# Kernel tuning notes

Hardware: AMD Instinct MI355X
Metric: run time of the kernel (lower is better)

## Reference

```python
import jax, jax.numpy as jnp
import numpy as np

N_NODES = 100000


def gcn_conv(x, edge_index, W, b):
    """PyG-style GCNConv: h = D^-1/2 (A+I) D^-1/2 (x W) + b."""
    n = x.shape[0]
    loop = jnp.arange(n)
    src = jnp.concatenate([edge_index[0], loop])  # [E+N]
    dst = jnp.concatenate([edge_index[1], loop])  # [E+N]
    # degree computed on destination nodes (PyG gcn_norm with self-loops)
    deg = jnp.zeros((n,), x.dtype).at[dst].add(1.0)
    dinv = jnp.where(deg > 0, jax.lax.rsqrt(deg), 0.0)
    norm = dinv[src] * dinv[dst]  # [E+N]
    h = x @ W  # [n, out]
    msg = h[src] * norm[:, None]  # gather + scale
    out = jax.ops.segment_sum(msg, dst, num_segments=n)  # scatter-add
    return out + b


def setup_inputs() -> dict:
    key = jax.random.key(0)
    ks = jax.random.split(key, 8)
    F_in, H, C = 64, 64, 32
    x = jax.random.normal(ks[0], (N_NODES, F_in), dtype=jnp.float32)
    edge_index = jax.random.randint(ks[1], (2, 1200000), 0, N_NODES, dtype=jnp.int64)
    W1 = jax.random.normal(ks[2], (F_in, H), dtype=jnp.float32) / np.sqrt(F_in)
    b1 = jnp.zeros((H,), jnp.float32)
    W2 = jax.random.normal(ks[3], (H, H), dtype=jnp.float32) / np.sqrt(H)
    b2 = jnp.zeros((H,), jnp.float32)
    Wc = jax.random.normal(ks[4], (H, C), dtype=jnp.float32) / np.sqrt(H)
    bc = jnp.zeros((C,), jnp.float32)
    return {"x": x, "edge_index": edge_index, "W1": W1, "b1": b1,
            "W2": W2, "b2": b2, "Wc": Wc, "bc": bc}


def reference(x, edge_index, W1, b1, W2, b2, Wc, bc):
    h = jnp.tanh(gcn_conv(x, edge_index, W1, b1))
    h = jnp.tanh(gcn_conv(h, edge_index, W2, b2))
    out = h @ Wc + bc
    return (out, h)
```

## Files before the change

### kernel.cpp

```cpp
#include <hip/hip_runtime.h>
#include <hip/hip_bf16.h>
#include <stdint.h>

#define CB_SHIFT 8
#define CB_NODES 256
#define CAP 3584
#define NBINS 512
#define PT 4096

static __device__ inline uint16_t f2bf(float f) {
    union { float f; uint32_t u; } v; v.f = f;
    uint32_t r = v.u + 0x7FFFu + ((v.u >> 16) & 1u);
    return (uint16_t)(r >> 16);
}
static __device__ inline float bflo(uint32_t u) {
    union { uint32_t u; float f; } v; v.u = u << 16; return v.f;
}
static __device__ inline float bfhi(uint32_t u) {
    union { uint32_t u; float f; } v; v.u = u & 0xFFFF0000u; return v.f;
}
static __device__ inline float bfu(uint16_t u) {
    union { uint32_t u; float f; } v; v.u = ((uint32_t)u) << 16; return v.f;
}
static __device__ inline float tanh_fast(float x) {
    x = fminf(fmaxf(x, -20.f), 20.f);
    float e = __expf(2.f * x);
    return fmaf(-2.f, __builtin_amdgcn_rcpf(e + 1.f), 1.f);
}

__global__ __launch_bounds__(256) void k_init(const uint32_t* __restrict__ e, int E,
                                              int* __restrict__ flag, int* __restrict__ gcur,
                                              int* __restrict__ dhist) {
    int t = threadIdx.x;
    dhist[t] = 0;
    gcur[t] = 0;
    gcur[256 + t] = 0;
    if (t < 64) {
        int cnt = E < 1024 ? E : 1024;
        int nz = 0;
        for (int i = t; i < cnt; i += 64) nz |= (e[2 * i + 1] != 0u);
        int any = __any(nz);
        if (t == 0) *flag = any ? 0 : 1;
    }
}

__global__ __launch_bounds__(256) void k_part(const uint32_t* __restrict__ e, int E,
                                              const int* __restrict__ flag,
                                              int* __restrict__ gcur,
                                              uint32_t* __restrict__ parts) {
    __shared__ int sh_hist[NBINS], sh_off[NBINS], sh_base[NBINS], pw[4];
    __shared__ uint32_t sh_buf[PT];
    __shared__ uint16_t sh_bkt[PT];
    int t = threadIdx.x;
    int tile0 = blockIdx.x * PT;
    int is64 = *flag;
    sh_hist[t] = 0;
    sh_hist[256 + t] = 0;
    __syncthreads();

    uint32_t rec[16]; int cb[16], rank[16];
    const uint2* e2p = (const uint2*)e;
    for (int j = 0; j < 16; ++j) {
        int idx = tile0 + j * 256 + t;
        cb[j] = -1;
        if (idx < E) {
            uint32_t s, d;
            if (is64) { s = e2p[idx].x; d = e2p[E + idx].x; }
            else      { s = e[idx];     d = e[E + idx]; }
            rec[j] = (s << CB_SHIFT) | (d & (CB_NODES - 1));
            cb[j] = (int)(d >> CB_SHIFT);
            rank[j] = atomicAdd(&sh_hist[cb[j]], 1);
        }
    }
    __syncthreads();
    int c0 = sh_hist[2 * t], c1 = sh_hist[2 * t + 1];
    int s2 = c0 + c1;
    int incl = s2;
    {
        int lane = t & 63;
        for (int o = 1; o < 64; o <<= 1) {
            int v = __shfl_up(incl, o);
            if (lane >= o) incl += v;
        }
        if (lane == 63) pw[t >> 6] = incl;
    }
    __syncthreads();
    if (t == 0) {
        int r = 0;
        for (int k = 0; k < 4; ++k) { int v = pw[k]; pw[k] = r; r += v; }
    }
    __syncthreads();
    {
        int ex = pw[t >> 6] + incl - s2;
        sh_off[2 * t] = ex;
        sh_off[2 * t + 1] = ex + c0;
        sh_base[2 * t]     = c0 ? atomicAdd(&gcur[2 * t], c0) : 0;
        sh_base[2 * t + 1] = c1 ? atomicAdd(&gcur[2 * t + 1], c1) : 0;
    }
    __syncthreads();
    for (int j = 0; j < 16; ++j) {
        if (cb[j] >= 0) {
            int slot = sh_off[cb[j]] + rank[j];
            sh_buf[slot] = rec[j];
            sh_bkt[slot] = (uint16_t)cb[j];
        }
    }
    __syncthreads();
    int total = min(PT, E - tile0);
    for (int i = t; i < total; i += 256) {
        int b = sh_bkt[i];
        int dest = sh_base[b] + (i - sh_off[b]);
        parts[(size_t)b * CAP + dest] = sh_buf[i];
    }
}

__global__ __launch_bounds__(512) void k_build(const uint32_t* __restrict__ parts,
                                               const int* __restrict__ gcur,
                                               float* __restrict__ dinv,
                                               int* __restrict__ rowbeg,
                                               int* __restrict__ rowend,
                                               uint32_t* __restrict__ col,
                                               int* __restrict__ dhist, int N) {
    __shared__ int hist[CB_NODES], cur[CB_NODES], dh[256], wsum4[4];
    __shared__ uint32_t sbuf[CAP];
    int t = threadIdx.x, cb = blockIdx.x;
    if (t < 256) { hist[t] = 0; dh[t] = 0; }
    __syncthreads();
    int cnt = gcur[cb];
    const uint32_t* rp = parts + (size_t)cb * CAP;
    for (int i = t; i < cnt; i += 512) atomicAdd(&hist[rp[i] & (CB_NODES - 1)], 1);
    __syncthreads();
    int h = 0, incl = 0;
    if (t < 256) {
        h = hist[t];
        int lane = t & 63;
        incl = h;
        for (int o = 1; o < 64; o <<= 1) {
            int v = __shfl_up(incl, o);
            if (lane >= o) incl += v;
        }
        if (lane == 63) wsum4[t >> 6] = incl;
    }
    __syncthreads();
    if (t == 0) {
        int r = 0;
        for (int k = 0; k < 4; ++k) { int v = wsum4[k]; wsum4[k] = r; r += v; }
    }
    __syncthreads();
    if (t < 256) {
        int ex = wsum4[t >> 6] + incl - h;
        cur[t] = ex;
        int n = cb * CB_NODES + t;
        int base = cb * CAP;
        if (n < N) {
            rowbeg[n] = base + ex;
            rowend[n] = base + ex + h;
            dinv[n] = rsqrtf((float)(h + 1));
            atomicAdd(&dh[min(h, 255)], 1);
        }
    }
    __syncthreads();
    if (t < 256 && dh[t]) atomicAdd(&dhist[t], dh[t]);
    for (int i = t; i < cnt; i += 512) {
        uint32_t rec = rp[i];
        int pos = atomicAdd(&cur[rec & (CB_NODES - 1)], 1);
        sbuf[pos] = rec >> CB_SHIFT;
    }
    __syncthreads();
    int base = cb * CAP;
    for (int i = t; i < cnt; i += 512) col[base + i] = sbuf[i];
}

__global__ __launch_bounds__(256) void k_dscan(const int* __restrict__ dhist,
                                               int* __restrict__ dcur) {
    __shared__ int sd[256];
    int t = threadIdx.x;
    int v = dhist[t];
    sd[t] = v; __syncthreads();
    for (int o = 1; o < 256; o <<= 1) {
        int x = (t >= o) ? sd[t - o] : 0;
        __syncthreads();
        sd[t] += x;
        __syncthreads();
    }
    dcur[t] = sd[t] - v;
}

__global__ __launch_bounds__(1024) void k_dperm(const int* __restrict__ rowbeg,
                                                const int* __restrict__ rowend,
                                                const float* __restrict__ dinv,
                                                int* __restrict__ dcur,
                                                int4* __restrict__ perm4, int N) {
    __shared__ int lh[256], lbase[256];
    int t = threadIdx.x;
    if (t < 256) lh[t] = 0;
    __syncthreads();
    int n = blockIdx.x * 1024 + t;
    int c = 0, rank = 0, beg = 0, deg = 0;
    if (n < N) {
        beg = rowbeg[n];
        deg = rowend[n] - beg;
        c = min(deg, 255);
        rank = atomicAdd(&lh[c], 1);
    }
    __syncthreads();
    if (t < 256 && lh[t]) lbase[t] = atomicAdd(&dcur[t], lh[t]);
    __syncthreads();
    if (n < N) {
        int pos = lbase[c] + rank;
        perm4[(N - 1) - pos] = make_int4(beg, deg, n, __float_as_int(dinv[n]));
    }
}

template<int ABF16>
__global__ __launch_bounds__(256) void k_gemm(const void* __restrict__ Ap,
                                              const float* __restrict__ W,
                                              const float* __restrict__ dinv,
                                              uint16_t* __restrict__ out, int N) {
    __shared__ __align__(16) float xT[64 * 68];
    __shared__ __align__(16) float Wl[64 * 64];
    int t = threadIdx.x;
#pragma unroll
    for (int j = 0; j < 16; ++j) Wl[j * 256 + t] = W[j * 256 + t];
    int n0 = blockIdx.x * 64;
    int nvalid = min(64, N - n0);
#pragma unroll
    for (int j = 0; j < 4; ++j) {
        int flat = j * 256 + t;
        int node = flat >> 4;
        int k4 = (flat & 15) * 4;
        float4 v = make_float4(0.f, 0.f, 0.f, 0.f);
        if (node < nvalid) {
            if (ABF16) {
                ushort4 u = *((const ushort4*)Ap + ((size_t)(n0 + node) * 16 + (k4 >> 2)));
                v = make_float4(bfu(u.x), bfu(u.y), bfu(u.z), bfu(u.w));
            } else {
                v = *(const float4*)((const float*)Ap + (size_t)(n0 + node) * 64 + k4);
            }
        }
        xT[(k4 + 0) * 68 + node] = v.x;
        xT[(k4 + 1) * 68 + node] = v.y;
        xT[(k4 + 2) * 68 + node] = v.z;
        xT[(k4 + 3) * 68 + node] = v.w;
    }
    __syncthreads();
    int ng = t >> 4, cg = t & 15;
    float acc[4][4] = {};
#pragma unroll 8
    for (int k = 0; k < 64; ++k) {
        float4 a = *(const float4*)&xT[k * 68 + 4 * ng];
        float4 b = *(const float4*)&Wl[k * 64 + 4 * cg];
        float av[4] = {a.x, a.y, a.z, a.w};
        float bv[4] = {b.x, b.y, b.z, b.w};
#pragma unroll
        for (int i = 0; i < 4; ++i)
#pragma unroll
            for (int j = 0; j < 4; ++j) acc[i][j] = fmaf(av[i], bv[j], acc[i][j]);
    }
#pragma unroll
    for (int i = 0; i < 4; ++i) {
        int ln = 4 * ng + i;
        if (ln < nvalid) {
            int n = n0 + ln;
            float dv = dinv[n];
            ushort4 o;
            o.x = f2bf(acc[i][0] * dv);
            o.y = f2bf(acc[i][1] * dv);
            o.z = f2bf(acc[i][2] * dv);
            o.w = f2bf(acc[i][3] * dv);
            *(ushort4*)&out[(size_t)n * 64 + 4 * cg] = o;
        }
    }
}

template<int OBF16>
__global__ __launch_bounds__(512) void k_agg(const uint16_t* __restrict__ h,
                                             const int4* __restrict__ perm4,
                                             const uint32_t* __restrict__ col,
                                             const float* __restrict__ bias,
                                             void* __restrict__ out, int N) {
    int t = threadIdx.x;
    int lane = t & 63, wid = t >> 6;
    int sub  = (lane >> 3) & 1;
    int g = lane & 7;
    const uint4* hp = (const uint4*)h;
    float bv[4];
#pragma unroll
    for (int j = 0; j < 4; ++j) bv[j] = bias[g * 8 + sub * 4 + j];
    int slot = lane >> 4;
    int idx = (blockIdx.x * 8 + wid) * 4 + slot;
    bool valid = idx < N;
    int4 pi = make_int4(0, 0, 0, 0);
    if (valid) pi = perm4[idx];
    int rs = pi.x, deg = valid ? pi.y : 0, n = pi.z;
    float di = __int_as_float(pi.w);
    int m = deg;
#pragma unroll
    for (int o = 1; o < 64; o <<= 1) m = max(m, __shfl_xor(m, o));
    int trips = (m + 1) >> 1;
    float acc[8] = {};
#pragma unroll 8
    for (int it = 0; it < trips; ++it) {
        int e = 2 * it + sub;
        if (e < deg) {
            int src = (int)col[rs + e];
            uint4 v = hp[(size_t)src * 8 + g];
            acc[0] += bflo(v.x); acc[1] += bfhi(v.x);
            acc[2] += bflo(v.y); acc[3] += bfhi(v.y);
            acc[4] += bflo(v.z); acc[5] += bfhi(v.z);
            acc[6] += bflo(v.w); acc[7] += bfhi(v.w);
        }
    }
#pragma unroll
    for (int j = 0; j < 8; ++j) acc[j] += __shfl_xor(acc[j], 8);
    if (valid) {
        float s0 = sub ? acc[4] : acc[0];
        float s1 = sub ? acc[5] : acc[1];
        float s2 = sub ? acc[6] : acc[2];
        float s3 = sub ? acc[7] : acc[3];
        uint2 v = *(const uint2*)&h[(size_t)n * 64 + g * 8 + sub * 4];
        float hn0 = bflo(v.x), hn1 = bfhi(v.x), hn2 = bflo(v.y), hn3 = bfhi(v.y);
        float r0 = tanh_fast(di * (s0 + hn0) + bv[0]);
        float r1 = tanh_fast(di * (s1 + hn1) + bv[1]);
        float r2 = tanh_fast(di * (s2 + hn2) + bv[2]);
        float r3 = tanh_fast(di * (s3 + hn3) + bv[3]);
        if (OBF16) {
            ushort4 ob;
            ob.x = f2bf(r0); ob.y = f2bf(r1); ob.z = f2bf(r2); ob.w = f2bf(r3);
            *(ushort4*)&((uint16_t*)out)[(size_t)n * 64 + g * 8 + sub * 4] = ob;
        } else {
            __align__(16) float o[4] = {r0, r1, r2, r3};
            *(float4*)&((float*)out)[(size_t)n * 64 + g * 8 + sub * 4] = *(float4*)&o[0];
        }
    }
}

__global__ __launch_bounds__(256) void k_cls(const float* __restrict__ A,
                                             const float* __restrict__ W,
                                             const float* __restrict__ bc,
                                             float* __restrict__ out, int N) {
    __shared__ __align__(16) float xT[64 * 68];
    __shared__ __align__(16) float Wl[64 * 32];
    int t = threadIdx.x;
#pragma unroll
    for (int j = 0; j < 8; ++j) Wl[j * 256 + t] = W[j * 256 + t];
    int n0 = blockIdx.x * 64;
    int nvalid = min(64, N - n0);
#pragma unroll
    for (int j = 0; j < 4; ++j) {
        int flat = j * 256 + t;
        int node = flat >> 4;
        int k4 = (flat & 15) * 4;
        float4 v = make_float4(0.f, 0.f, 0.f, 0.f);
        if (node < nvalid) v = *(const float4*)&A[(size_t)(n0 + node) * 64 + k4];
        xT[(k4 + 0) * 68 + node] = v.x;
        xT[(k4 + 1) * 68 + node] = v.y;
        xT[(k4 + 2) * 68 + node] = v.z;
        xT[(k4 + 3) * 68 + node] = v.w;
    }
    __syncthreads();
    int ng = t >> 4, cg = t & 15;
    float acc[4][2] = {};
#pragma unroll 8
    for (int k = 0; k < 64; ++k) {
        float4 a = *(const float4*)&xT[k * 68 + 4 * ng];
        float2 b = *(const float2*)&Wl[k * 32 + 2 * cg];
        float av[4] = {a.x, a.y, a.z, a.w};
#pragma unroll
        for (int i = 0; i < 4; ++i) {
            acc[i][0] = fmaf(av[i], b.x, acc[i][0]);
            acc[i][1] = fmaf(av[i], b.y, acc[i][1]);
        }
    }
    float2 bcv = *(const float2*)&bc[2 * cg];
#pragma unroll
    for (int i = 0; i < 4; ++i) {
        int ln = 4 * ng + i;
        if (ln < nvalid) {
            int n = n0 + ln;
            float2 o = make_float2(acc[i][0] + bcv.x, acc[i][1] + bcv.y);
            *(float2*)&out[(size_t)n * 32 + 2 * cg] = o;
        }
    }
}

extern "C" void kernel_launch(void* const* d_in, const int* in_sizes, int n_in,
                              void* d_out, int out_size, void* d_ws, size_t ws_size,
                              hipStream_t stream) {
    const float*    x     = (const float*)d_in[0];
    const uint32_t* edges = (const uint32_t*)d_in[1];
    const float*    W1    = (const float*)d_in[2];
    const float*    b1    = (const float*)d_in[3];
    const float*    W2    = (const float*)d_in[4];
    const float*    b2    = (const float*)d_in[5];
    const float*    Wc    = (const float*)d_in[6];
    const float*    bc    = (const float*)d_in[7];

    const int N   = in_sizes[0] / 64;
    const int E   = in_sizes[1] / 2;
    const int NBC = (N + CB_NODES - 1) >> CB_SHIFT;
    const int NTG = (N + 63) / 64;
    const int NTP = (E + PT - 1) / PT;
    const int NAG = (N + 31) / 32;
    const int NDP = (N + 1023) / 1024;

    char* w = (char*)d_ws;
    size_t off = 0;
    auto alloc = [&](size_t bytes) {
        void* p = w + off;
        off = (off + bytes + 255) & ~(size_t)255;
        return p;
    };
    int*      flag   = (int*)alloc(4);
    int*      gcur   = (int*)alloc(NBINS * 4);
    int*      dhist  = (int*)alloc(256 * 4);
    int*      dcur   = (int*)alloc(256 * 4);
    float*    dinv   = (float*)alloc((size_t)N * 4);
    uint32_t* parts  = (uint32_t*)alloc((size_t)NBC * CAP * 4);
    uint32_t* col    = (uint32_t*)alloc((size_t)NBC * CAP * 4);
    int*      rowbeg = (int*)alloc((size_t)N * 4);
    int*      rowend = (int*)alloc((size_t)N * 4);
    uint16_t* bufA   = (uint16_t*)alloc((size_t)N * 64 * 2);
    uint16_t* bufB   = (uint16_t*)alloc((size_t)N * 64 * 2);
    int4*     perm4  = (int4*)parts;

    float* outc = (float*)d_out;
    float* hfin = outc + (size_t)N * 32;

    hipLaunchKernelGGL(k_init, dim3(1), dim3(256), 0, stream, edges, E, flag, gcur, dhist);
    hipLaunchKernelGGL(k_part, dim3(NTP), dim3(256), 0, stream, edges, E, flag, gcur, parts);
    hipLaunchKernelGGL(k_build, dim3(NBC), dim3(512), 0, stream, parts, gcur, dinv, rowbeg, rowend, col, dhist, N);
    hipLaunchKernelGGL(k_dscan, dim3(1), dim3(256), 0, stream, dhist, dcur);
    hipLaunchKernelGGL(k_dperm, dim3(NDP), dim3(1024), 0, stream, rowbeg, rowend, dinv, dcur, perm4, N);

    hipLaunchKernelGGL(HIP_KERNEL_NAME(k_gemm<0>), dim3(NTG), dim3(256), 0, stream,
                       (const void*)x, W1, dinv, bufA, N);
    hipLaunchKernelGGL(HIP_KERNEL_NAME(k_agg<1>), dim3(NAG), dim3(512), 0, stream,
                       bufA, perm4, col, b1, (void*)bufB, N);
    hipLaunchKernelGGL(HIP_KERNEL_NAME(k_gemm<1>), dim3(NTG), dim3(256), 0, stream,
                       (const void*)bufB, W2, dinv, bufA, N);
    hipLaunchKernelGGL(HIP_KERNEL_NAME(k_agg<0>), dim3(NAG), dim3(512), 0, stream,
                       bufA, perm4, col, b2, (void*)hfin, N);
    hipLaunchKernelGGL(k_cls, dim3(NTG), dim3(256), 0, stream, hfin, Wc, bc, outc, N);
}
```

Baseline: 243.7 us.

## Fuse classifier matmul into second aggregation kernel and widen partition blocks

The separate classifier kernel is removed. The second aggregation kernel now stages each node's final tanh output in shared memory and computes the 64x32 classifier product with bias directly, using Wc loaded into LDS. This avoids re-reading the N x 64 fp32 hidden output from global memory and saves one launch, at the cost of extra LDS use and per-block Wc loads. Separately, the edge partition kernel moves to 512 threads with one histogram bin per thread and a two-level shuffle scan.

Result: faster. 236.2 us (-3.1%).

```diff
diff --git a/kernel.cpp b/kernel.cpp
--- a/kernel.cpp
+++ b/kernel.cpp
@@ -44,24 +44,24 @@
     }
 }
 
-__global__ __launch_bounds__(256) void k_part(const uint32_t* __restrict__ e, int E,
+__global__ __launch_bounds__(512) void k_part(const uint32_t* __restrict__ e, int E,
                                               const int* __restrict__ flag,
                                               int* __restrict__ gcur,
                                               uint32_t* __restrict__ parts) {
-    __shared__ int sh_hist[NBINS], sh_off[NBINS], sh_base[NBINS], pw[4];
+    __shared__ int sh_hist[NBINS], sh_off[NBINS], sh_base[NBINS], pw[8];
     __shared__ uint32_t sh_buf[PT];
     __shared__ uint16_t sh_bkt[PT];
     int t = threadIdx.x;
     int tile0 = blockIdx.x * PT;
     int is64 = *flag;
     sh_hist[t] = 0;
-    sh_hist[256 + t] = 0;
-    __syncthreads();
-
-    uint32_t rec[16]; int cb[16], rank[16];
+    __syncthreads();
+
+    uint32_t rec[8]; int cb[8], rank[8];
     const uint2* e2p = (const uint2*)e;
-    for (int j = 0; j < 16; ++j) {
-        int idx = tile0 + j * 256 + t;
+#pragma unroll
+    for (int j = 0; j < 8; ++j) {
+        int idx = tile0 + j * 512 + t;
         cb[j] = -1;
         if (idx < E) {
             uint32_t s, d;
@@ -73,32 +73,34 @@
         }
     }
     __syncthreads();
-    int c0 = sh_hist[2 * t], c1 = sh_hist[2 * t + 1];
-    int s2 = c0 + c1;
-    int incl = s2;
+    int c = sh_hist[t];
+    int lane = t & 63, w = t >> 6;
+    int incl = c;
+    for (int o = 1; o < 64; o <<= 1) {
+        int v = __shfl_up(incl, o);
+        if (lane >= o) incl += v;
+    }
+    if (lane == 63) pw[w] = incl;
+    __syncthreads();
+    if (t < 8) {
+        int v = pw[t];
+        int inc2 = v;
+#pragma unroll
+        for (int o = 1; o < 8; o <<= 1) {
+            int u = __shfl_up(inc2, o);
+            if (t >= o) inc2 += u;
+        }
+        pw[t] = inc2 - v;
+    }
+    __syncthreads();
     {
-        int lane = t & 63;
-        for (int o = 1; o < 64; o <<= 1) {
-            int v = __shfl_up(incl, o);
-            if (lane >= o) incl += v;
-        }
-        if (lane == 63) pw[t >> 6] = incl;
-    }
-    __syncthreads();
-    if (t == 0) {
-        int r = 0;
-        for (int k = 0; k < 4; ++k) { int v = pw[k]; pw[k] = r; r += v; }
-    }
-    __syncthreads();
-    {
-        int ex = pw[t >> 6] + incl - s2;
-        sh_off[2 * t] = ex;
-        sh_off[2 * t + 1] = ex + c0;
-        sh_base[2 * t]     = c0 ? atomicAdd(&gcur[2 * t], c0) : 0;
-        sh_base[2 * t + 1] = c1 ? atomicAdd(&gcur[2 * t + 1], c1) : 0;
-    }
-    __syncthreads();
-    for (int j = 0; j < 16; ++j) {
+        int ex = pw[w] + incl - c;
+        sh_off[t] = ex;
+        sh_base[t] = c ? atomicAdd(&gcur[t], c) : 0;
+    }
+    __syncthreads();
+#pragma unroll
+    for (int j = 0; j < 8; ++j) {
         if (cb[j] >= 0) {
             int slot = sh_off[cb[j]] + rank[j];
             sh_buf[slot] = rec[j];
@@ -107,7 +109,7 @@
     }
     __syncthreads();
     int total = min(PT, E - tile0);
-    for (int i = t; i < total; i += 256) {
+    for (int i = t; i < total; i += 512) {
         int b = sh_bkt[i];
         int dest = sh_base[b] + (i - sh_off[b]);
         parts[(size_t)b * CAP + dest] = sh_buf[i];
@@ -273,13 +275,23 @@
     }
 }
 
-template<int OBF16>
+template<int OBF16, int CLS>
 __global__ __launch_bounds__(512) void k_agg(const uint16_t* __restrict__ h,
                                              const int4* __restrict__ perm4,
                                              const uint32_t* __restrict__ col,
                                              const float* __restrict__ bias,
-                                             void* __restrict__ out, int N) {
-    int t = threadIdx.x;
+                                             void* __restrict__ out,
+                                             const float* __restrict__ Wc,
+                                             const float* __restrict__ bc,
+                                             float* __restrict__ outc, int N) {
+    __shared__ __align__(16) float WcL[CLS ? 64 * 32 : 1];
+    __shared__ __align__(16) float hstage[CLS ? 8 : 1][4][64];
+    int t = threadIdx.x;
+    if (CLS) {
+#pragma unroll
+        for (int j = 0; j < 4; ++j) WcL[j * 512 + t] = Wc[j * 512 + t];
+        __syncthreads();
+    }
     int lane = t & 63, wid = t >> 6;
     int sub  = (lane >> 3) & 1;
     int g = lane & 7;
@@ -332,54 +344,28 @@
             __align__(16) float o[4] = {r0, r1, r2, r3};
             *(float4*)&((float*)out)[(size_t)n * 64 + g * 8 + sub * 4] = *(float4*)&o[0];
         }
-    }
-}
-
-__global__ __launch_bounds__(256) void k_cls(const float* __restrict__ A,
-                                             const float* __restrict__ W,
-                                             const float* __restrict__ bc,
-                                             float* __restrict__ out, int N) {
-    __shared__ __align__(16) float xT[64 * 68];
-    __shared__ __align__(16) float Wl[64 * 32];
-    int t = threadIdx.x;
-#pragma unroll
-    for (int j = 0; j < 8; ++j) Wl[j * 256 + t] = W[j * 256 + t];
-    int n0 = blockIdx.x * 64;
-    int nvalid = min(64, N - n0);
-#pragma unroll
-    for (int j = 0; j < 4; ++j) {
-        int flat = j * 256 + t;
-        int node = flat >> 4;
-        int k4 = (flat & 15) * 4;
-        float4 v = make_float4(0.f, 0.f, 0.f, 0.f);
-        if (node < nvalid) v = *(const float4*)&A[(size_t)(n0 + node) * 64 + k4];
-        xT[(k4 + 0) * 68 + node] = v.x;
-        xT[(k4 + 1) * 68 + node] = v.y;
-        xT[(k4 + 2) * 68 + node] = v.z;
-        xT[(k4 + 3) * 68 + node] = v.w;
-    }
-    __syncthreads();
-    int ng = t >> 4, cg = t & 15;
-    float acc[4][2] = {};
-#pragma unroll 8
-    for (int k = 0; k < 64; ++k) {
-        float4 a = *(const float4*)&xT[k * 68 + 4 * ng];
-        float2 b = *(const float2*)&Wl[k * 32 + 2 * cg];
-        float av[4] = {a.x, a.y, a.z, a.w};
-#pragma unroll
-        for (int i = 0; i < 4; ++i) {
-            acc[i][0] = fmaf(av[i], b.x, acc[i][0]);
-            acc[i][1] = fmaf(av[i], b.y, acc[i][1]);
-        }
-    }
-    float2 bcv = *(const float2*)&bc[2 * cg];
-#pragma unroll
-    for (int i = 0; i < 4; ++i) {
-        int ln = 4 * ng + i;
-        if (ln < nvalid) {
-            int n = n0 + ln;
-            float2 o = make_float2(acc[i][0] + bcv.x, acc[i][1] + bcv.y);
-            *(float2*)&out[(size_t)n * 32 + 2 * cg] = o;
+        if (CLS)
+            *(float4*)&hstage[wid][slot][g * 8 + sub * 4] = make_float4(r0, r1, r2, r3);
+    }
+    if (CLS) {
+        int q = lane & 15;
+        if (valid) {
+            float a0 = 0.f, a1 = 0.f;
+#pragma unroll
+            for (int k = 0; k < 64; k += 4) {
+                float4 hv = *(const float4*)&hstage[wid][slot][k];
+                float2 w0 = *(const float2*)&WcL[(k + 0) * 32 + 2 * q];
+                float2 w1 = *(const float2*)&WcL[(k + 1) * 32 + 2 * q];
+                float2 w2 = *(const float2*)&WcL[(k + 2) * 32 + 2 * q];
+                float2 w3 = *(const float2*)&WcL[(k + 3) * 32 + 2 * q];
+                a0 = fmaf(hv.x, w0.x, a0); a1 = fmaf(hv.x, w0.y, a1);
+                a0 = fmaf(hv.y, w1.x, a0); a1 = fmaf(hv.y, w1.y, a1);
+                a0 = fmaf(hv.z, w2.x, a0); a1 = fmaf(hv.z, w2.y, a1);
+                a0 = fmaf(hv.w, w3.x, a0); a1 = fmaf(hv.w, w3.y, a1);
+            }
+            float2 bcv = *(const float2*)&bc[2 * q];
+            float2 o = make_float2(a0 + bcv.x, a1 + bcv.y);
+            *(float2*)&outc[(size_t)n * 32 + 2 * q] = o;
         }
     }
 }
@@ -428,18 +414,18 @@
     float* hfin = outc + (size_t)N * 32;
 
     hipLaunchKernelGGL(k_init, dim3(1), dim3(256), 0, stream, edges, E, flag, gcur, dhist);
-    hipLaunchKernelGGL(k_part, dim3(NTP), dim3(256), 0, stream, edges, E, flag, gcur, parts);
+    hipLaunchKernelGGL(k_part, dim3(NTP), dim3(512), 0, stream, edges, E, flag, gcur, parts);
     hipLaunchKernelGGL(k_build, dim3(NBC), dim3(512), 0, stream, parts, gcur, dinv, rowbeg, rowend, col, dhist, N);
     hipLaunchKernelGGL(k_dscan, dim3(1), dim3(256), 0, stream, dhist, dcur);
     hipLaunchKernelGGL(k_dperm, dim3(NDP), dim3(1024), 0, stream, rowbeg, rowend, dinv, dcur, perm4, N);
 
     hipLaunchKernelGGL(HIP_KERNEL_NAME(k_gemm<0>), dim3(NTG), dim3(256), 0, stream,
                        (const void*)x, W1, dinv, bufA, N);
-    hipLaunchKernelGGL(HIP_KERNEL_NAME(k_agg<1>), dim3(NAG), dim3(512), 0, stream,
-                       bufA, perm4, col, b1, (void*)bufB, N);
+    hipLaunchKernelGGL(HIP_KERNEL_NAME(k_agg<1, 0>), dim3(NAG), dim3(512), 0, stream,
+                       bufA, perm4, col, b1, (void*)bufB, (const float*)nullptr,
+                       (const float*)nullptr, (float*)nullptr, N);
     hipLaunchKernelGGL(HIP_KERNEL_NAME(k_gemm<1>), dim3(NTG), dim3(256), 0, stream,
                        (const void*)bufB, W2, dinv, bufA, N);
-    hipLaunchKernelGGL(HIP_KERNEL_NAME(k_agg<0>), dim3(NAG), dim3(512), 0, stream,
-                       bufA, perm4, col, b2, (void*)hfin, N);
-    hipLaunchKernelGGL(k_cls, dim3(NTG), dim3(256), 0, stream, hfin, Wc, bc, outc, N);
-}
+    hipLaunchKernelGGL(HIP_KERNEL_NAME(k_agg<0, 1>), dim3(NAG), dim3(512), 0, stream,
+                       bufA, perm4, col, b2, (void*)hfin, Wc, bc, outc, N);
+}
```
